# Performance work log

Measured on AMD Instinct MI355X. Metric: run time of the kernel, lower is better.

The kernel has to match this reference:

```python
import jax, jax.numpy as jnp
import numpy as np

N_NODES = 50000
N_EDGES = 1600000
IN_F, H_F, N_C = 128, 128, 16
NEG_SLOPE = 0.2  # DGL GATConv default


def setup_inputs() -> dict:
    key = jax.random.key(0)
    ks = jax.random.split(key, 12)
    def w(k, shape, fan_in):
        return jax.random.normal(k, shape, jnp.float32) / np.float32(np.sqrt(fan_in))
    return {
        "feat": jax.random.normal(ks[0], (N_NODES, IN_F), jnp.float32),
        "src": jax.random.randint(ks[1], (N_EDGES,), 0, N_NODES, dtype=jnp.int32),
        "dst": jax.random.randint(ks[2], (N_EDGES,), 0, N_NODES, dtype=jnp.int32),
        "W1": w(ks[3], (IN_F, H_F), IN_F), "al1": w(ks[4], (H_F,), H_F), "ar1": w(ks[5], (H_F,), H_F), "b1": jnp.zeros((H_F,), jnp.float32),
        "W2": w(ks[6], (H_F, H_F), H_F), "al2": w(ks[7], (H_F,), H_F), "ar2": w(ks[8], (H_F,), H_F), "b2": jnp.zeros((H_F,), jnp.float32),
        "W3": w(ks[9], (H_F, N_C), H_F), "al3": w(ks[10], (N_C,), N_C), "ar3": w(ks[11], (N_C,), N_C), "b3": jnp.zeros((N_C,), jnp.float32),
    }


def _gat_layer(h, src, dst, W, al, ar, b):
    # DGL GATConv (1 head): ft = W h; e_ij = LeakyReLU(a_l.ft_src + a_r.ft_dst);
    # alpha = edge_softmax over incoming edges of dst; out = sum alpha * ft_src + bias
    ft = h @ W                                   # [N, out]
    el = ft @ al                                 # [N]
    er = ft @ ar                                 # [N]
    e = jax.nn.leaky_relu(el[src] + er[dst], negative_slope=NEG_SLOPE)  # [E]
    emax = jax.ops.segment_max(e, dst, num_segments=N_NODES)
    emax = jnp.where(jnp.isfinite(emax), emax, 0.0)  # guard isolated nodes
    ex = jnp.exp(e - emax[dst])                  # [E]
    esum = jax.ops.segment_sum(ex, dst, num_segments=N_NODES)  # [N]
    agg = jax.ops.segment_sum(ex[:, None] * ft[src], dst, num_segments=N_NODES)  # [N, out]
    out = agg / jnp.where(esum > 0, esum, 1.0)[:, None] + b
    return jax.nn.relu(out)


def reference(feat, src, dst, W1, al1, ar1, b1, W2, al2, ar2, b2, W3, al3, ar3, b3):
    h = _gat_layer(feat, src, dst, W1, al1, ar1, b1)
    h = _gat_layer(h, src, dst, W2, al2, ar2, b2)
    h = _gat_layer(h, src, dst, W3, al3, ar3, b3)
    return h  # [N_NODES, N_C]
```

## Files before the change

### kernel.cpp

```cpp
#include <hip/hip_runtime.h>
#include <hip/hip_bf16.h>

#define NN 50000
#define NE 1600000
#define FF 128
#define CC 16
#define NB ((NN + 63) / 64)
#define NBLK 128
#define CH ((NE + NBLK - 1) / NBLK)

using bf16 = __hip_bfloat16;
using bf16x8 = __attribute__((ext_vector_type(8))) short;
using f32x4  = __attribute__((ext_vector_type(4))) float;

static __device__ __forceinline__ float ldf(const void* p, int i, int isbf){
    return isbf ? __bfloat162float(((const bf16*)p)[i]) : ((const float*)p)[i];
}
static __device__ __forceinline__ float bflo(unsigned u){
    union{unsigned x; float f;} c; c.x = u << 16; return c.f;
}
static __device__ __forceinline__ float bfhi(unsigned u){
    union{unsigned x; float f;} c; c.x = u & 0xFFFF0000u; return c.f;
}
static __device__ __forceinline__ float rdlanef(float v, int l){
    return __int_as_float(__builtin_amdgcn_readlane(__float_as_int(v), l));
}
static __device__ __forceinline__ unsigned short f2bfu(float v){
    bf16 b = __float2bfloat16(v);
    union{bf16 b; unsigned short u;} c; c.b = b; return c.u;
}

__global__ __launch_bounds__(256) void k_detect(const unsigned short* __restrict__ u,
                                                int* __restrict__ flag){
    int t = threadIdx.x;
    unsigned short lo = u[2 * t];
    int e = (lo >> 7) & 0xFF;
    int sane = (e >= 117 && e <= 137) ? 1 : 0;
    __shared__ int cnt;
    if (t == 0) cnt = 0;
    __syncthreads();
    atomicAdd(&cnt, sane);
    __syncthreads();
    if (t == 0) *flag = (cnt >= 128) ? 1 : 0;
}

__global__ __launch_bounds__(256) void k_zero(int* __restrict__ p, int n){
    int i = blockIdx.x * 256 + threadIdx.x;
    if (i < n) p[i] = 0;
}

__global__ __launch_bounds__(256) void k_wprep(const void* __restrict__ W1, const void* __restrict__ W2,
                                               const int* __restrict__ dflag, unsigned short* __restrict__ wtg){
    const int isbf = *dflag;
    int idx = blockIdx.x * 256 + threadIdx.x;
    int l = idx >> 14;
    int e = idx & 16383;
    int f = e >> 7, k = e & 127;
    const void* W = l ? W2 : W1;
    wtg[idx] = f2bfu(ldf(W, k * FF + f, isbf));
}


__global__ __launch_bounds__(256) void k_bcount(const int* __restrict__ dst, int* __restrict__ bcounts,
                                                int* __restrict__ bh){
    __shared__ int hist[NB];
    const int t = threadIdx.x, b = blockIdx.x;
    for (int i = t; i < NB; i += 256) hist[i] = 0;
    __syncthreads();
    const int beg = b * CH, end = (beg + CH < NE) ? beg + CH : NE;
    for (int i = beg + t; i < end; i += 256){
        int d = dst[i];
        if ((unsigned)d >= NN) d = 0;
        atomicAdd(&hist[d >> 6], 1);
    }
    __syncthreads();
    for (int k = t; k < NB; k += 256){
        int v = hist[k];
        bh[k * NBLK + b] = v;
        if (v) atomicAdd(&bcounts[k], v);
    }
}

__global__ __launch_bounds__(256) void k_bscan(const int* __restrict__ bcounts, int* __restrict__ bbase,
                                               int* __restrict__ rowptr){
    __shared__ int s[256];
    const int t = threadIdx.x;
    constexpr int PT = (NB + 255) / 256;
    int loc[PT];
    int sum = 0;
    #pragma unroll
    for (int i = 0; i < PT; i++){
        int idx = t * PT + i;
        int v = (idx < NB) ? bcounts[idx] : 0;
        loc[i] = sum;
        sum += v;
    }
    s[t] = sum; __syncthreads();
    for (int off = 1; off < 256; off <<= 1){
        int x = (t >= off) ? s[t - off] : 0;
        __syncthreads();
        s[t] += x;
        __syncthreads();
    }
    int base = (t > 0) ? s[t - 1] : 0;
    #pragma unroll
    for (int i = 0; i < PT; i++){
        int idx = t * PT + i;
        if (idx < NB) bbase[idx] = base + loc[i];
    }
    if (t == 255){
        bbase[NB] = s[255];
        rowptr[NN] = s[255];
    }
}

__global__ __launch_bounds__(256) void k_boffset(const int* __restrict__ bbase, int* __restrict__ bh){
    int k = blockIdx.x * 4 + (threadIdx.x >> 6);
    int lane = threadIdx.x & 63;
    if (k >= NB) return;
    int v0 = bh[k * NBLK + 2 * lane];
    int v1 = bh[k * NBLK + 2 * lane + 1];
    int s = v0 + v1;
    #pragma unroll
    for (int off = 1; off < 64; off <<= 1){
        int x = __shfl_up(s, off);
        if (lane >= off) s += x;
    }
    int base = bbase[k] + s - (v0 + v1);
    bh[k * NBLK + 2 * lane]     = base;
    bh[k * NBLK + 2 * lane + 1] = base + v0;
}

__global__ __launch_bounds__(256) void k_bucket(const int* __restrict__ src, const int* __restrict__ dst,
                                                const int* __restrict__ bh, unsigned* __restrict__ bpairs){
    __shared__ int cur[NB];
    const int t = threadIdx.x, b = blockIdx.x;
    for (int k = t; k < NB; k += 256) cur[k] = bh[k * NBLK + b];
    __syncthreads();
    const int beg = b * CH, end = (beg + CH < NE) ? beg + CH : NE;
    for (int i = beg + t; i < end; i += 256){
        int s = src[i];
        int d = dst[i];
        if ((unsigned)s >= NN) s = 0;
        if ((unsigned)d >= NN) d = 0;
        int p = atomicAdd(&cur[d >> 6], 1);
        if ((unsigned)p < NE) bpairs[p] = (unsigned)s | ((unsigned)(d & 63) << 16);
    }
}

__global__ __launch_bounds__(256) void k_bsort(const unsigned* __restrict__ bpairs, const int* __restrict__ bbase,
                                               int* __restrict__ rowptr, int* __restrict__ csrsrc){
    __shared__ int cnt[64];
    __shared__ int cur[64];
    const int t = threadIdx.x;
    const int b = blockIdx.x;
    const int base = bbase[b];
    const int endb = bbase[b + 1];
    if (t < 64) cnt[t] = 0;
    __syncthreads();
    for (int i = base + t; i < endb; i += 256)
        atomicAdd(&cnt[bpairs[i] >> 16], 1);
    __syncthreads();
    if (t < 64){
        int v = cnt[t];
        int inc = v;
        #pragma unroll
        for (int off = 1; off < 64; off <<= 1){
            int x = __shfl_up(inc, off);
            if (t >= off) inc += x;
        }
        int excl = inc - v;
        cur[t] = excl;
        int d = b * 64 + t;
        if (d < NN) rowptr[d] = base + excl;
    }
    __syncthreads();
    for (int i = base + t; i < endb; i += 256){
        unsigned pr = bpairs[i];
        int p = atomicAdd(&cur[pr >> 16], 1);
        csrsrc[base + p] = (int)(pr & 0xFFFFu);
    }
}


#define XPAD 136

template<bool XDYN>
__global__ __launch_bounds__(256) void k_mgemm(const void* __restrict__ X, const unsigned short* __restrict__ wtg,
                                               const void* __restrict__ al, const void* __restrict__ ar,
                                               const int* __restrict__ dflag, bf16* __restrict__ ft,
                                               float* __restrict__ el, float* __restrict__ er){
    __shared__ unsigned short xs[64 * XPAD];
    __shared__ unsigned short wt[128 * XPAD];
    const int isbf = *dflag;
    const int t  = threadIdx.x;
    const int n0 = blockIdx.x * 64;

    for (int i2 = t; i2 < 8192; i2 += 256){
        unsigned v = ((const unsigned*)wtg)[i2];
        int r = i2 >> 6, c2 = (i2 & 63) * 2;
        *(unsigned*)&wt[r * XPAD + c2] = v;
    }
    for (int i2 = t; i2 < 4096; i2 += 256){
        int r = i2 >> 6, c2 = (i2 & 63) * 2;
        int n = n0 + r;
        float v0 = 0.f, v1 = 0.f;
        if (n < NN){
            if (XDYN){ v0 = ldf(X, n * FF + c2, isbf); v1 = ldf(X, n * FF + c2 + 1, isbf); }
            else     { v0 = ((const float*)X)[n * FF + c2]; v1 = ((const float*)X)[n * FF + c2 + 1]; }
        }
        unsigned pk = (unsigned)f2bfu(v0) | ((unsigned)f2bfu(v1) << 16);
        *(unsigned*)&xs[r * XPAD + c2] = pk;
    }
    __syncthreads();

    const int wv = t >> 6;
    const int lane = t & 63;
    const int quad = lane >> 4;
    const int mcol = lane & 15;

    bf16x8 afr[4];
    const unsigned short* xrow = &xs[(wv * 16 + mcol) * XPAD + quad * 8];
    #pragma unroll
    for (int kt = 0; kt < 4; kt++)
        afr[kt] = *(const bf16x8*)(xrow + kt * 32);

    float elp[4] = {0.f,0.f,0.f,0.f}, erp[4] = {0.f,0.f,0.f,0.f};

    #pragma unroll
    for (int f = 0; f < 8; f++){
        f32x4 acc = {0.f, 0.f, 0.f, 0.f};
        const unsigned short* wrow = &wt[(f * 16 + mcol) * XPAD + quad * 8];
        #pragma unroll
        for (int kt = 0; kt < 4; kt++){
            bf16x8 bfr = *(const bf16x8*)(wrow + kt * 32);
            acc = __builtin_amdgcn_mfma_f32_16x16x32_bf16(afr[kt], bfr, acc, 0, 0, 0);
        }
        int col = f * 16 + mcol;
        float alv = ldf(al, col, isbf);
        float arv = ldf(ar, col, isbf);
        #pragma unroll
        for (int reg = 0; reg < 4; reg++){
            int node = n0 + wv * 16 + quad * 4 + reg;
            float v = acc[reg];
            if (node < NN) ft[node * FF + col] = __float2bfloat16(v);
            elp[reg] += v * alv;
            erp[reg] += v * arv;
        }
    }

    #pragma unroll
    for (int reg = 0; reg < 4; reg++){
        float pl = elp[reg], pr = erp[reg];
        #pragma unroll
        for (int off = 1; off < 16; off <<= 1){
            pl += __shfl_xor(pl, off);
            pr += __shfl_xor(pr, off);
        }
        int node = n0 + wv * 16 + quad * 4 + reg;
        if (mcol == 0 && node < NN){ el[node] = pl; er[node] = pr; }
    }
}


__global__ __launch_bounds__(256) void k_gemm3(const float* __restrict__ X, const void* __restrict__ W,
                                               const void* __restrict__ al, const void* __restrict__ ar,
                                               const int* __restrict__ dflag, float* __restrict__ ft,
                                               float* __restrict__ el, float* __restrict__ er){
    constexpr int BN = 16;
    __shared__ float xs[FF][BN + 1];
    const int isbf = *dflag;
    const int t  = threadIdx.x;
    const int n0 = blockIdx.x * BN;

    for (int idx = t; idx < BN * FF; idx += 256){
        int r = idx >> 7;
        int c = idx & 127;
        int n = n0 + r;
        xs[c][r] = (n < NN) ? X[n * FF + c] : 0.f;
    }
    __syncthreads();

    const int tx = t & 15;
    const int rg = t >> 4;
    float acc = 0.f;
    if (isbf){
        const bf16* Wb = (const bf16*)W;
        for (int k = 0; k < FF; k++)
            acc += __bfloat162float(Wb[k * CC + tx]) * xs[k][rg];
    } else {
        const float* Wf = (const float*)W;
        for (int k = 0; k < FF; k++)
            acc += Wf[k * CC + tx] * xs[k][rg];
    }

    int n = n0 + rg;
    if (n < NN) ft[n * CC + tx] = acc;

    float alv = ldf(al, tx, isbf);
    float arv = ldf(ar, tx, isbf);
    float pl = acc * alv, pr = acc * arv;
    #pragma unroll
    for (int off = 1; off < 16; off <<= 1){
        pl += __shfl_xor(pl, off);
        pr += __shfl_xor(pr, off);
    }
    if (tx == 0 && n < NN){ el[n] = pl; er[n] = pr; }
}


__global__ __launch_bounds__(256) void k_agg128(const void* __restrict__ ftv, const float* __restrict__ el,
                                                const float* __restrict__ er, const int* __restrict__ rowptr,
                                                const int* __restrict__ csrsrc, const void* __restrict__ bias,
                                                const int* __restrict__ dflag, float* __restrict__ outp){
    const int isbf = *dflag;
    int lane = threadIdx.x & 63;
    int n = blockIdx.x * 4 + (threadIdx.x >> 6);
    if (n >= NN) return;
    int beg = rowptr[n], end = rowptr[n + 1];
    beg = (beg < 0) ? 0 : (beg > NE ? NE : beg);
    end = (end < beg) ? beg : (end > NE ? NE : end);
    int deg = end - beg;
    float erd = er[n];

    float m = -3.4e38f;
    int   s_c = 0;
    float e_c = 0.f;
    for (int i = beg + lane; i < end; i += 64){
        int s = csrsrc[i];
        if ((unsigned)s >= NN) s = 0;
        float e = el[s] + erd;
        e = (e >= 0.f) ? e : 0.2f * e;
        if (i < beg + 64){ s_c = s; e_c = e; }
        m = fmaxf(m, e);
    }
    #pragma unroll
    for (int off = 32; off; off >>= 1) m = fmaxf(m, __shfl_xor(m, off));

    int jmax = (deg < 64) ? deg : 64;
    float w_c = (lane < jmax) ? __expf(e_c - m) : 0.f;
    float lsum = w_c;
    #pragma unroll
    for (int off = 32; off; off >>= 1) lsum += __shfl_xor(lsum, off);

    const unsigned* ftb = (const unsigned*)ftv;
    float acc0 = 0.f, acc1 = 0.f;
    int j = 0;
    if (jmax >= 8){
        float w[8]; unsigned u[8];
        #pragma unroll
        for (int q = 0; q < 8; q++){
            int s = __builtin_amdgcn_readlane(s_c, q);
            w[q] = rdlanef(w_c, q);
            u[q] = (ftb + s * 64)[lane];
        }
        for (j = 8; j + 8 <= jmax; j += 8){
            float wn[8]; unsigned un[8];
            #pragma unroll
            for (int q = 0; q < 8; q++){
                int s = __builtin_amdgcn_readlane(s_c, j + q);
                wn[q] = rdlanef(w_c, j + q);
                un[q] = (ftb + s * 64)[lane];
            }
            #pragma unroll
            for (int q = 0; q < 8; q++){
                acc0 += w[q] * bflo(u[q]);
                acc1 += w[q] * bfhi(u[q]);
                w[q] = wn[q]; u[q] = un[q];
            }
        }
        #pragma unroll
        for (int q = 0; q < 8; q++){
            acc0 += w[q] * bflo(u[q]);
            acc1 += w[q] * bfhi(u[q]);
        }
    }
    for (; j < jmax; ++j){
        int s = __builtin_amdgcn_readlane(s_c, j);
        float w = rdlanef(w_c, j);
        unsigned u = (ftb + s * 64)[lane];
        acc0 += w * bflo(u); acc1 += w * bfhi(u);
    }
    for (int i = beg + 64; i < end; ++i){
        int s = csrsrc[i];
        if ((unsigned)s >= NN) s = 0;
        float e = el[s] + erd;
        e = (e >= 0.f) ? e : 0.2f * e;
        float w = __expf(e - m);
        unsigned u = (ftb + s * 64)[lane];
        lsum += w;
        acc0 += w * bflo(u); acc1 += w * bfhi(u);
    }
    float inv = 1.f / ((lsum > 0.f) ? lsum : 1.f);
    float2 o;
    o.x = fmaxf(acc0 * inv + ldf(bias, 2 * lane,     isbf), 0.f);
    o.y = fmaxf(acc1 * inv + ldf(bias, 2 * lane + 1, isbf), 0.f);
    ((float2*)outp)[n * 64 + lane] = o;
}


__global__ __launch_bounds__(256) void k_agg16(const float* __restrict__ ftv, const float* __restrict__ el,
                                               const float* __restrict__ er, const int* __restrict__ rowptr,
                                               const int* __restrict__ csrsrc, const void* __restrict__ bias,
                                               const int* __restrict__ dflag, void* __restrict__ outp){
    const int isbf = *dflag;
    int lane = threadIdx.x & 63;
    int n = blockIdx.x * 4 + (threadIdx.x >> 6);
    if (n >= NN) return;
    int beg = rowptr[n], end = rowptr[n + 1];
    beg = (beg < 0) ? 0 : (beg > NE ? NE : beg);
    end = (end < beg) ? beg : (end > NE ? NE : end);
    int deg = end - beg;
    float erd = er[n];

    float m = -3.4e38f;
    int   s_c = 0;
    float e_c = 0.f;
    for (int i = beg + lane; i < end; i += 64){
        int s = csrsrc[i];
        if ((unsigned)s >= NN) s = 0;
        float e = el[s] + erd;
        e = (e >= 0.f) ? e : 0.2f * e;
        if (i < beg + 64){ s_c = s; e_c = e; }
        m = fmaxf(m, e);
    }
    #pragma unroll
    for (int off = 32; off; off >>= 1) m = fmaxf(m, __shfl_xor(m, off));

    int jmax = (deg < 64) ? deg : 64;
    float w_c = (lane < jmax) ? __expf(e_c - m) : 0.f;
    float lsum = w_c;
    #pragma unroll
    for (int off = 32; off; off >>= 1) lsum += __shfl_xor(lsum, off);

    const float4* ftq = (const float4*)ftv;
    const int g   = lane >> 2;
    const int fl2 = lane & 3;
    int nbatch = (jmax + 15) >> 4;
    float wq[4]; float4 uq[4];
    #pragma unroll
    for (int q = 0; q < 4; q++){
        int eidx = (q * 16 + g) & 63;
        int s = __shfl(s_c, eidx);
        wq[q] = (q < nbatch) ? __shfl(w_c, eidx) : 0.f;
        uq[q] = ftq[(unsigned)s * 4 + fl2];
    }
    float a4[4] = {0.f,0.f,0.f,0.f};
    #pragma unroll
    for (int q = 0; q < 4; q++){
        a4[0] += wq[q] * uq[q].x;
        a4[1] += wq[q] * uq[q].y;
        a4[2] += wq[q] * uq[q].z;
        a4[3] += wq[q] * uq[q].w;
    }
    for (int i = beg + 64; i < end; ++i){
        int s = csrsrc[i];
        if ((unsigned)s >= NN) s = 0;
        float e = el[s] + erd;
        e = (e >= 0.f) ? e : 0.2f * e;
        float w = __expf(e - m);
        lsum += w;
        if (g == 0){
            float4 u = ftq[(unsigned)s * 4 + fl2];
            a4[0] += w * u.x; a4[1] += w * u.y; a4[2] += w * u.z; a4[3] += w * u.w;
        }
    }
    #pragma unroll
    for (int i = 0; i < 4; i++){
        a4[i] += __shfl_xor(a4[i], 4);
        a4[i] += __shfl_xor(a4[i], 8);
        a4[i] += __shfl_xor(a4[i], 16);
        a4[i] += __shfl_xor(a4[i], 32);
    }
    float inv = 1.f / ((lsum > 0.f) ? lsum : 1.f);
    if (lane < 4){
        float o0 = fmaxf(a4[0] * inv + ldf(bias, fl2 * 4 + 0, isbf), 0.f);
        float o1 = fmaxf(a4[1] * inv + ldf(bias, fl2 * 4 + 1, isbf), 0.f);
        float o2 = fmaxf(a4[2] * inv + ldf(bias, fl2 * 4 + 2, isbf), 0.f);
        float o3 = fmaxf(a4[3] * inv + ldf(bias, fl2 * 4 + 3, isbf), 0.f);
        if (isbf){
            uint2 pk;
            pk.x = (unsigned)f2bfu(o0) | ((unsigned)f2bfu(o1) << 16);
            pk.y = (unsigned)f2bfu(o2) | ((unsigned)f2bfu(o3) << 16);
            ((uint2*)outp)[n * 4 + fl2] = pk;
        } else {
            float4 o; o.x = o0; o.y = o1; o.z = o2; o.w = o3;
            ((float4*)outp)[n * 4 + fl2] = o;
        }
    }
}


static size_t align256(size_t x){ return (x + 255) & ~(size_t)255; }

extern "C" void kernel_launch(void* const* d_in, const int* in_sizes, int n_in,
                              void* d_out, int out_size, void* d_ws, size_t ws_size,
                              hipStream_t stream) {
    const void* feat = d_in[0];
    const int*  src  = (const int*)d_in[1];
    const int*  dst  = (const int*)d_in[2];
    const void* W1 = d_in[3];
    const void* al1= d_in[4];
    const void* ar1= d_in[5];
    const void* b1 = d_in[6];
    const void* W2 = d_in[7];
    const void* al2= d_in[8];
    const void* ar2= d_in[9];
    const void* b2 = d_in[10];
    const void* W3 = d_in[11];
    const void* al3= d_in[12];
    const void* ar3= d_in[13];
    const void* b3 = d_in[14];

    char* p = (char*)d_ws;
    size_t off = 0;
    auto carve = [&](size_t bytes)->void*{
        void* r = p + off;
        off += align256(bytes);
        return r;
    };
    float* ftA   = (float*)carve((size_t)NN * FF * 4);
    float* hB    = (float*)carve((size_t)NN * FF * 4);
    float* el    = (float*)carve((size_t)NN * 4);
    float* er    = (float*)carve((size_t)NN * 4);
    int*   rowptr= (int*)  carve((size_t)(NN + 1) * 4);
    int*   csrsrc= (int*)  carve((size_t)NE * 4);
    int*   bcounts=(int*)  carve((size_t)NB * 4);
    int*   bbase  =(int*)  carve((size_t)(NB + 1) * 4);
    int*   bh     =(int*)  carve((size_t)NB * NBLK * 4);
    unsigned short* wtg = (unsigned short*)carve(2 * 16384 * 2);
    int*   dflag  =(int*)  carve(256);
    unsigned* bpairs = (unsigned*)hB;
    void*  ftb   = ftA;
    (void)ws_size; (void)n_in; (void)in_sizes; (void)out_size;

    dim3 b256(256);

    k_detect<<<dim3(1), b256, 0, stream>>>((const unsigned short*)feat, dflag);
    k_wprep<<<dim3(128), b256, 0, stream>>>(W1, W2, dflag, wtg);

    k_zero<<<dim3((NB + 255) / 256), b256, 0, stream>>>(bcounts, NB);
    k_bcount<<<dim3(NBLK), b256, 0, stream>>>(dst, bcounts, bh);
    k_bscan<<<dim3(1), b256, 0, stream>>>(bcounts, bbase, rowptr);
    k_boffset<<<dim3((NB + 3) / 4), b256, 0, stream>>>(bbase, bh);
    k_bucket<<<dim3(NBLK), b256, 0, stream>>>(src, dst, bh, bpairs);
    k_bsort<<<dim3(NB), b256, 0, stream>>>(bpairs, bbase, rowptr, csrsrc);

    const int mg_grid   = (NN + 63) / 64;
    const int g3_grid   = (NN + 15) / 16;
    const int node_grid = (NN + 3) / 4;

    k_mgemm<true><<<dim3(mg_grid), b256, 0, stream>>>(feat, wtg, al1, ar1, dflag, (bf16*)ftb, el, er);
    k_agg128<<<dim3(node_grid), b256, 0, stream>>>(ftb, el, er, rowptr, csrsrc, b1, dflag, hB);

    k_mgemm<false><<<dim3(mg_grid), b256, 0, stream>>>(hB, wtg + 16384, al2, ar2, dflag, (bf16*)ftb, el, er);
    k_agg128<<<dim3(node_grid), b256, 0, stream>>>(ftb, el, er, rowptr, csrsrc, b2, dflag, hB);

    k_gemm3<<<dim3(g3_grid), b256, 0, stream>>>(hB, W3, al3, ar3, dflag, (float*)ftb, el, er);
    k_agg16<<<dim3(node_grid), b256, 0, stream>>>((const float*)ftb, el, er, rowptr, csrsrc, b3, dflag, d_out);
}
```

Before: 366.8 us.

## Use MFMA for layer-3 GEMM and double bucketing block count

Replaces the scalar fp32 layer-3 GEMM (128->16) with an MFMA bf16 kernel over 64-node tiles, using a pre-transposed bf16 copy of W3 built in the weight-prep kernel. Separately raises the edge-bucketing block count from 128 to 256 and adapts the offset scan to four values per lane. The MFMA path rounds layer-3 inputs to bf16, which lowers precision; more bucketing blocks mean more parallelism but a larger histogram table.

```diff
diff --git a/kernel.cpp b/kernel.cpp
--- a/kernel.cpp
+++ b/kernel.cpp
@@ -6,7 +6,7 @@
 #define FF 128
 #define CC 16
 #define NB ((NN + 63) / 64)
-#define NBLK 128
+#define NBLK 256
 #define CH ((NE + NBLK - 1) / NBLK)
 
 using bf16 = __hip_bfloat16;
@@ -50,14 +50,21 @@
 }
 
 __global__ __launch_bounds__(256) void k_wprep(const void* __restrict__ W1, const void* __restrict__ W2,
-                                               const int* __restrict__ dflag, unsigned short* __restrict__ wtg){
+                                               const void* __restrict__ W3, const int* __restrict__ dflag,
+                                               unsigned short* __restrict__ wtg){
     const int isbf = *dflag;
     int idx = blockIdx.x * 256 + threadIdx.x;
-    int l = idx >> 14;
-    int e = idx & 16383;
-    int f = e >> 7, k = e & 127;
-    const void* W = l ? W2 : W1;
-    wtg[idx] = f2bfu(ldf(W, k * FF + f, isbf));
+    if (idx < 32768){
+        int l = idx >> 14;
+        int e = idx & 16383;
+        int f = e >> 7, k = e & 127;
+        const void* W = l ? W2 : W1;
+        wtg[idx] = f2bfu(ldf(W, k * FF + f, isbf));
+    } else {
+        int e = idx - 32768;
+        int f = e >> 7, k = e & 127;
+        wtg[idx] = f2bfu(ldf(W3, k * CC + f, isbf));
+    }
 }
 
 
@@ -118,17 +125,25 @@
     int k = blockIdx.x * 4 + (threadIdx.x >> 6);
     int lane = threadIdx.x & 63;
     if (k >= NB) return;
-    int v0 = bh[k * NBLK + 2 * lane];
-    int v1 = bh[k * NBLK + 2 * lane + 1];
-    int s = v0 + v1;
+    int v[4];
+    int s = 0;
+    #pragma unroll
+    for (int i = 0; i < 4; i++){
+        v[i] = bh[k * NBLK + 4 * lane + i];
+        s += v[i];
+    }
+    int tot = s;
     #pragma unroll
     for (int off = 1; off < 64; off <<= 1){
         int x = __shfl_up(s, off);
         if (lane >= off) s += x;
     }
-    int base = bbase[k] + s - (v0 + v1);
-    bh[k * NBLK + 2 * lane]     = base;
-    bh[k * NBLK + 2 * lane + 1] = base + v0;
+    int run = bbase[k] + s - tot;
+    #pragma unroll
+    for (int i = 0; i < 4; i++){
+        bh[k * NBLK + 4 * lane + i] = run;
+        run += v[i];
+    }
 }
 
 __global__ __launch_bounds__(256) void k_bucket(const int* __restrict__ src, const int* __restrict__ dst,
@@ -263,49 +278,64 @@
 }
 
 
-__global__ __launch_bounds__(256) void k_gemm3(const float* __restrict__ X, const void* __restrict__ W,
-                                               const void* __restrict__ al, const void* __restrict__ ar,
-                                               const int* __restrict__ dflag, float* __restrict__ ft,
-                                               float* __restrict__ el, float* __restrict__ er){
-    constexpr int BN = 16;
-    __shared__ float xs[FF][BN + 1];
+__global__ __launch_bounds__(256) void k_mgemm3(const float* __restrict__ X, const unsigned short* __restrict__ wt3g,
+                                                const void* __restrict__ al, const void* __restrict__ ar,
+                                                const int* __restrict__ dflag, float* __restrict__ ft,
+                                                float* __restrict__ el, float* __restrict__ er){
+    __shared__ unsigned short xs[64 * XPAD];
+    __shared__ unsigned short wt[16 * XPAD];
     const int isbf = *dflag;
     const int t  = threadIdx.x;
-    const int n0 = blockIdx.x * BN;
-
-    for (int idx = t; idx < BN * FF; idx += 256){
-        int r = idx >> 7;
-        int c = idx & 127;
+    const int n0 = blockIdx.x * 64;
+
+    for (int i2 = t; i2 < 1024; i2 += 256){
+        unsigned v = ((const unsigned*)wt3g)[i2];
+        int r = i2 >> 6, c2 = (i2 & 63) * 2;
+        *(unsigned*)&wt[r * XPAD + c2] = v;
+    }
+    for (int i2 = t; i2 < 4096; i2 += 256){
+        int r = i2 >> 6, c2 = (i2 & 63) * 2;
         int n = n0 + r;
-        xs[c][r] = (n < NN) ? X[n * FF + c] : 0.f;
-    }
-    __syncthreads();
-
-    const int tx = t & 15;
-    const int rg = t >> 4;
-    float acc = 0.f;
-    if (isbf){
-        const bf16* Wb = (const bf16*)W;
-        for (int k = 0; k < FF; k++)
-            acc += __bfloat162float(Wb[k * CC + tx]) * xs[k][rg];
-    } else {
-        const float* Wf = (const float*)W;
-        for (int k = 0; k < FF; k++)
-            acc += Wf[k * CC + tx] * xs[k][rg];
-    }
-
-    int n = n0 + rg;
-    if (n < NN) ft[n * CC + tx] = acc;
-
-    float alv = ldf(al, tx, isbf);
-    float arv = ldf(ar, tx, isbf);
-    float pl = acc * alv, pr = acc * arv;
-    #pragma unroll
-    for (int off = 1; off < 16; off <<= 1){
-        pl += __shfl_xor(pl, off);
-        pr += __shfl_xor(pr, off);
-    }
-    if (tx == 0 && n < NN){ el[n] = pl; er[n] = pr; }
+        float v0 = 0.f, v1 = 0.f;
+        if (n < NN){
+            v0 = X[n * FF + c2];
+            v1 = X[n * FF + c2 + 1];
+        }
+        unsigned pk = (unsigned)f2bfu(v0) | ((unsigned)f2bfu(v1) << 16);
+        *(unsigned*)&xs[r * XPAD + c2] = pk;
+    }
+    __syncthreads();
+
+    const int wv = t >> 6;
+    const int lane = t & 63;
+    const int quad = lane >> 4;
+    const int mcol = lane & 15;
+
+    f32x4 acc = {0.f, 0.f, 0.f, 0.f};
+    const unsigned short* xrow = &xs[(wv * 16 + mcol) * XPAD + quad * 8];
+    const unsigned short* wrow = &wt[mcol * XPAD + quad * 8];
+    #pragma unroll
+    for (int kt = 0; kt < 4; kt++){
+        bf16x8 afr = *(const bf16x8*)(xrow + kt * 32);
+        bf16x8 bfr = *(const bf16x8*)(wrow + kt * 32);
+        acc = __builtin_amdgcn_mfma_f32_16x16x32_bf16(afr, bfr, acc, 0, 0, 0);
+    }
+
+    float alv = ldf(al, mcol, isbf);
+    float arv = ldf(ar, mcol, isbf);
+    #pragma unroll
+    for (int reg = 0; reg < 4; reg++){
+        int node = n0 + wv * 16 + quad * 4 + reg;
+        float v = acc[reg];
+        if (node < NN) ft[node * CC + mcol] = v;
+        float pl = v * alv, pr = v * arv;
+        #pragma unroll
+        for (int off = 1; off < 16; off <<= 1){
+            pl += __shfl_xor(pl, off);
+            pr += __shfl_xor(pr, off);
+        }
+        if (mcol == 0 && node < NN){ el[node] = pl; er[node] = pr; }
+    }
 }
 
 
@@ -528,7 +558,7 @@
     int*   bcounts=(int*)  carve((size_t)NB * 4);
     int*   bbase  =(int*)  carve((size_t)(NB + 1) * 4);
     int*   bh     =(int*)  carve((size_t)NB * NBLK * 4);
-    unsigned short* wtg = (unsigned short*)carve(2 * 16384 * 2);
+    unsigned short* wtg = (unsigned short*)carve((size_t)34816 * 2);
     int*   dflag  =(int*)  carve(256);
     unsigned* bpairs = (unsigned*)hB;
     void*  ftb   = ftA;
@@ -537,7 +567,7 @@
     dim3 b256(256);
 
     k_detect<<<dim3(1), b256, 0, stream>>>((const unsigned short*)feat, dflag);
-    k_wprep<<<dim3(128), b256, 0, stream>>>(W1, W2, dflag, wtg);
+    k_wprep<<<dim3(136), b256, 0, stream>>>(W1, W2, W3, dflag, wtg);
 
     k_zero<<<dim3((NB + 255) / 256), b256, 0, stream>>>(bcounts, NB);
     k_bcount<<<dim3(NBLK), b256, 0, stream>>>(dst, bcounts, bh);
@@ -547,7 +577,6 @@
     k_bsort<<<dim3(NB), b256, 0, stream>>>(bpairs, bbase, rowptr, csrsrc);
 
     const int mg_grid   = (NN + 63) / 64;
-    const int g3_grid   = (NN + 15) / 16;
     const int node_grid = (NN + 3) / 4;
 
     k_mgemm<true><<<dim3(mg_grid), b256, 0, stream>>>(feat, wtg, al1, ar1, dflag, (bf16*)ftb, el, er);
@@ -556,6 +585,6 @@
     k_mgemm<false><<<dim3(mg_grid), b256, 0, stream>>>(hB, wtg + 16384, al2, ar2, dflag, (bf16*)ftb, el, er);
     k_agg128<<<dim3(node_grid), b256, 0, stream>>>(ftb, el, er, rowptr, csrsrc, b2, dflag, hB);
 
-    k_gemm3<<<dim3(g3_grid), b256, 0, stream>>>(hB, W3, al3, ar3, dflag, (float*)ftb, el, er);
+    k_mgemm3<<<dim3(mg_grid), b256, 0, stream>>>(hB, wtg + 32768, al3, ar3, dflag, (float*)ftb, el, er);
     k_agg16<<<dim3(node_grid), b256, 0, stream>>>((const float*)ftb, el, er, rowptr, csrsrc, b3, dflag, d_out);
 }
```

Measured after the change: 340.4 us. -7.2%, faster.
